# Optimization experiments

Measured on AMD Instinct MI355X. Metric: run time of the kernel, lower is better.

The kernel has to match this reference:

```python
import jax, jax.numpy as jnp
import numpy as np

B, T, D, H = 2048, 512, 32, 64


def _gru_layer(x, W_ih, W_hh, b_ih, b_hh):
    # x: [B, T, Din]; W_ih: [3H, Din]; W_hh: [3H, H]; gate order r, z, n (PyTorch).
    xp = jnp.einsum('btd,gd->btg', x, W_ih) + b_ih  # precompute input projections [B,T,3H]

    def step(h, xt):
        gh = h @ W_hh.T + b_hh                      # [B,3H]
        ir, iz, inn = jnp.split(xt, 3, axis=-1)
        hr, hz, hn = jnp.split(gh, 3, axis=-1)
        r = jax.nn.sigmoid(ir + hr)
        z = jax.nn.sigmoid(iz + hz)
        n = jnp.tanh(inn + r * hn)
        h_new = (1.0 - z) * n + z * h
        return h_new, h_new

    h0 = jnp.zeros((x.shape[0], W_hh.shape[1]), dtype=x.dtype)
    _, ys = jax.lax.scan(step, h0, xp.transpose(1, 0, 2))  # ys: [T,B,H]
    return ys.transpose(1, 0, 2)                           # [B,T,H]


def setup_inputs() -> dict:
    key = jax.random.key(0)
    ks = jax.random.split(key, 12)
    s_in = 1.0 / np.sqrt(H)
    u = lambda k, shp: jax.random.uniform(k, shp, jnp.float32, -s_in, s_in)
    return {
        'x': jax.random.normal(ks[0], (B, T, D), jnp.float32),
        'W_ih0': u(ks[1], (3 * H, D)),  'W_hh0': u(ks[2], (3 * H, H)),
        'b_ih0': u(ks[3], (3 * H,)),    'b_hh0': u(ks[4], (3 * H,)),
        'W_ih1': u(ks[5], (3 * H, H)),  'W_hh1': u(ks[6], (3 * H, H)),
        'b_ih1': u(ks[7], (3 * H,)),    'b_hh1': u(ks[8], (3 * H,)),
        'fc_w': u(ks[9], (1, H)),       'fc_b': u(ks[10], (1,)),
    }


def reference(x, W_ih0, W_hh0, b_ih0, b_hh0, W_ih1, W_hh1, b_ih1, b_hh1, fc_w, fc_b):
    # 2-layer GRU (eval mode: inter-layer dropout is identity) + linear head on last step.
    h1 = _gru_layer(x, W_ih0, W_hh0, b_ih0, b_hh0)   # [B,T,H]
    h2 = _gru_layer(h1, W_ih1, W_hh1, b_ih1, b_hh1)  # [B,T,H]
    out = h2[:, -1, :] @ fc_w.T + fc_b               # [B,1]
    return out[:, 0]                                  # [B]
```

## Files before the change

kernel.cpp:

```cpp
#include <hip/hip_runtime.h>

#define Bsz  2048
#define Tlen 512
#define Din  32
#define Hd   64
#define BT   16
#define HS   72
#define BUFE 2048
#define CHUNK 16
#define XSTR  2064
#define XBUFB (BT * XSTR)

typedef _Float16 half8 __attribute__((ext_vector_type(8)));
typedef float    f32x4 __attribute__((ext_vector_type(4)));

#define MFMA(a, b, c) __builtin_amdgcn_mfma_f32_16x16x32_f16((a), (b), (c), 0, 0, 0)

__device__ __forceinline__ half8 load8s(const float* p, float s) {
    half8 r;
#pragma unroll
    for (int j = 0; j < 8; ++j) r[j] = (_Float16)(p[j] * s);
    return r;
}
__device__ __forceinline__ half8 cvt8(float4 a, float4 b) {
    half8 r;
    r[0] = (_Float16)a.x; r[1] = (_Float16)a.y; r[2] = (_Float16)a.z; r[3] = (_Float16)a.w;
    r[4] = (_Float16)b.x; r[5] = (_Float16)b.y; r[6] = (_Float16)b.z; r[7] = (_Float16)b.w;
    return r;
}

__device__ __forceinline__ void gate_update(const f32x4& gr, const f32x4& gz,
                                            const f32x4& anx, const f32x4& anh,
                                            float hst[4], _Float16* dst, bool wr) {
#pragma unroll
    for (int r = 0; r < 4; ++r) {
        float Er = __builtin_amdgcn_exp2f(gr[r]);
        float rr = __builtin_amdgcn_rcpf(1.0f + Er);
        float yy = anx[r] + rr * anh[r];
        float En = __builtin_amdgcn_exp2f(yy);
        float Ez = __builtin_amdgcn_exp2f(gz[r]);
        float num = Ez * (1.0f - En) + hst[r] * (1.0f + En);
        float den = (1.0f + Ez) * (1.0f + En);
        hst[r] = num * __builtin_amdgcn_rcpf(den);
        if (wr) dst[r * HS] = (_Float16)hst[r];
    }
}

__device__ __forceinline__ void stage_chunk(const float* __restrict__ x, char* xs,
                                            int wave, int lane, int b0, int t0, int p) {
#pragma unroll
    for (int j = 0; j < 4; ++j) {
        const int g  = wave * 4 + j;
        const int b  = g >> 1;
        const int hh = g & 1;
        const float* gp = x + (size_t)(b0 + b) * (Tlen * Din) + (size_t)t0 * Din
                            + hh * 256 + lane * 4;
        char* lp = xs + p * XBUFB + b * XSTR + hh * 1024 + lane * 16;
        __builtin_amdgcn_global_load_lds(
            (const __attribute__((address_space(1))) void*)gp,
            (__attribute__((address_space(3))) void*)lp, 16, 0, 0);
    }
}

__global__ __launch_bounds__(512, 2)
void gru_fused(const float* __restrict__ x,
               const float* __restrict__ Wih0, const float* __restrict__ Whh0,
               const float* __restrict__ bih0, const float* __restrict__ bhh0,
               const float* __restrict__ Wih1, const float* __restrict__ Whh1,
               const float* __restrict__ bih1, const float* __restrict__ bhh1,
               const float* __restrict__ fcw,  const float* __restrict__ fcb,
               float* __restrict__ out)
{
    __shared__ _Float16 arena[4 * BUFE];
    __shared__ __attribute__((aligned(16))) char xstage[2 * XBUFB];
    __shared__ float hfin[BT][Hd];

    const int tid  = threadIdx.x;
    const int lane = tid & 63;
    const int wave = tid >> 6;
    const int grp  = wave >> 2;
    const int wg   = wave & 3;
    const int m    = lane & 15;
    const int quad = lane >> 4;
    const int col  = (wg << 4) + m;
    const int b0   = blockIdx.x << 4;

    for (int idx = tid; idx < 4 * BUFE; idx += 512) arena[idx] = (_Float16)0.f;

    stage_chunk(x, xstage, wave, lane, b0, 0, 0);
    stage_chunk(x, xstage, wave, lane, b0, CHUNK, 1);

    const float sRZ = -1.44269504f;
    const float sN  = -2.88539008f;

    half8 wx[2][3], wh[2][3];
    float brz0, brz1, bin_, bhn_;

    if (grp == 0) {
        wx[0][0] = load8s(Wih0 + (      col) * Din + quad * 8, sRZ);
        wx[0][1] = load8s(Wih0 + ( 64 + col) * Din + quad * 8, sRZ);
        wx[0][2] = load8s(Wih0 + (128 + col) * Din + quad * 8, sN);
#pragma unroll
        for (int kb = 0; kb < 2; ++kb) {
            wh[kb][0] = load8s(Whh0 + (      col) * Hd + kb * 32 + quad * 8, sRZ);
            wh[kb][1] = load8s(Whh0 + ( 64 + col) * Hd + kb * 32 + quad * 8, sRZ);
            wh[kb][2] = load8s(Whh0 + (128 + col) * Hd + kb * 32 + quad * 8, sN);
        }
        brz0 = sRZ * (bih0[col] + bhh0[col]);
        brz1 = sRZ * (bih0[64 + col] + bhh0[64 + col]);
        bin_ = sN * bih0[128 + col];
        bhn_ = sN * bhh0[128 + col];
    } else {
#pragma unroll
        for (int kb = 0; kb < 2; ++kb) {
            wx[kb][0] = load8s(Wih1 + (      col) * Hd + kb * 32 + quad * 8, sRZ);
            wx[kb][1] = load8s(Wih1 + ( 64 + col) * Hd + kb * 32 + quad * 8, sRZ);
            wx[kb][2] = load8s(Wih1 + (128 + col) * Hd + kb * 32 + quad * 8, sN);
            wh[kb][0] = load8s(Whh1 + (      col) * Hd + kb * 32 + quad * 8, sRZ);
            wh[kb][1] = load8s(Whh1 + ( 64 + col) * Hd + kb * 32 + quad * 8, sRZ);
            wh[kb][2] = load8s(Whh1 + (128 + col) * Hd + kb * 32 + quad * 8, sN);
        }
        brz0 = sRZ * (bih1[col] + bhh1[col]);
        brz1 = sRZ * (bih1[64 + col] + bhh1[64 + col]);
        bin_ = sN * bih1[128 + col];
        bhn_ = sN * bhh1[128 + col];
    }

    const int rdoff = m * HS + quad * 8;
    const int xroff = m * XSTR + quad * 32;
    const int wroff = (quad * 4) * HS + col;
    float hst[4] = {0.f, 0.f, 0.f, 0.f};
    float4 xa, xb;
    __syncthreads();

    if (grp == 0) {
        const char* xr = xstage + xroff;
        xa = *(const float4*)xr; xb = *(const float4*)(xr + 16);
    }

#define STEP(I, RO, WO)                                                          \
  do {                                                                           \
    if (grp == 0) {                                                              \
      half8 ax = cvt8(xa, xb);                                                   \
      const _Float16* s1 = arena + (RO) + rdoff;                                 \
      half8 ah0 = *(const half8*)s1;                                             \
      half8 ah1 = *(const half8*)(s1 + 32);                                      \
      f32x4 arx = {brz0, brz0, brz0, brz0};                                      \
      f32x4 azx = {brz1, brz1, brz1, brz1};                                      \
      f32x4 anx = {bin_, bin_, bin_, bin_};                                      \
      f32x4 arh = {0.f,0.f,0.f,0.f}, azh = {0.f,0.f,0.f,0.f};                    \
      f32x4 anh = {bhn_, bhn_, bhn_, bhn_};                                      \
      arh = MFMA(ah0, wh[0][0], arh); arh = MFMA(ah1, wh[1][0], arh);            \
      azh = MFMA(ah0, wh[0][1], azh); azh = MFMA(ah1, wh[1][1], azh);            \
      anh = MFMA(ah0, wh[0][2], anh); anh = MFMA(ah1, wh[1][2], anh);            \
      arx = MFMA(ax, wx[0][0], arx);                                             \
      azx = MFMA(ax, wx[0][1], azx);                                             \
      anx = MFMA(ax, wx[0][2], anx);                                             \
      f32x4 gr = arx + arh, gz = azx + azh;                                      \
      gate_update(gr, gz, anx, anh, hst, arena + (WO) + wroff, true);            \
      { const int nx = ((I) + 1 < Tlen) ? (I) + 1 : (I);                         \
        const char* xr = xstage + ((nx >> 4) & 1) * XBUFB + (nx & 15) * 128      \
                         + xroff;                                                \
        xa = *(const float4*)xr; xb = *(const float4*)(xr + 16); }               \
    } else {                                                                     \
      const _Float16* s1 = arena + (RO) + rdoff;                    \
      const _Float16* s2 = s1 + 2 * BUFE;                           \
      half8 ax0 = *(const half8*)s1;                                             \
      half8 ax1 = *(const half8*)(s1 + 32);                                      \
      half8 ah0 = *(const half8*)s2;                                             \
      half8 ah1 = *(const half8*)(s2 + 32);                                      \
      f32x4 arx = {brz0, brz0, brz0, brz0};                                      \
      f32x4 azx = {brz1, brz1, brz1, brz1};                                      \
      f32x4 anx = {bin_, bin_, bin_, bin_};                                      \
      f32x4 arh = {0.f,0.f,0.f,0.f}, azh = {0.f,0.f,0.f,0.f};                    \
      f32x4 anh = {bhn_, bhn_, bhn_, bhn_};                                      \
      arx = MFMA(ax0, wx[0][0], arx); arx = MFMA(ax1, wx[1][0], arx);            \
      azx = MFMA(ax0, wx[0][1], azx); azx = MFMA(ax1, wx[1][1], azx);            \
      anx = MFMA(ax0, wx[0][2], anx); anx = MFMA(ax1, wx[1][2], anx);            \
      arh = MFMA(ah0, wh[0][0], arh); arh = MFMA(ah1, wh[1][0], arh);            \
      azh = MFMA(ah0, wh[0][1], azh); azh = MFMA(ah1, wh[1][1], azh);            \
      anh = MFMA(ah0, wh[0][2], anh); anh = MFMA(ah1, wh[1][2], anh);            \
      f32x4 gr = arx + arh, gz = azx + azh;                                      \
      gate_update(gr, gz, anx, anh, hst, arena + (2 * BUFE) + (WO) + wroff,      \
                  true);                                                         \
    }                                                                            \
    __syncthreads();                                                             \
  } while (0)

    if (grp == 0) {
        half8 ax = cvt8(xa, xb);
        f32x4 gr  = {brz0, brz0, brz0, brz0};
        f32x4 gz  = {brz1, brz1, brz1, brz1};
        f32x4 anx = {bin_, bin_, bin_, bin_};
        f32x4 anh = {bhn_, bhn_, bhn_, bhn_};
        gr  = MFMA(ax, wx[0][0], gr);
        gz  = MFMA(ax, wx[0][1], gz);
        anx = MFMA(ax, wx[0][2], anx);
        gate_update(gr, gz, anx, anh, hst, arena + 0 + wroff, true);
        const char* xr = xstage + 128 + xroff;
        xa = *(const float4*)xr; xb = *(const float4*)(xr + 16);
    }
    __syncthreads();

    for (int i = 1; i + 1 < Tlen; i += 2) {
        STEP(i, 0, BUFE);
        if (((i + 1) & (CHUNK - 1)) == 0 && (i + 1) < Tlen - CHUNK)
            stage_chunk(x, xstage, wave, lane, b0, i + 1 + CHUNK,
                        (((i + 1) >> 4) + 1) & 1);
        STEP(i + 1, BUFE, 0);
    }
    STEP(Tlen - 1, 0, BUFE);

    if (grp == 1) {
        const _Float16* s1 = arena + BUFE + rdoff;
        const _Float16* s2 = s1 + 2 * BUFE;
        half8 ax0 = *(const half8*)s1;
        half8 ax1 = *(const half8*)(s1 + 32);
        half8 ah0 = *(const half8*)s2;
        half8 ah1 = *(const half8*)(s2 + 32);
        f32x4 arx = {brz0, brz0, brz0, brz0};
        f32x4 azx = {brz1, brz1, brz1, brz1};
        f32x4 anx = {bin_, bin_, bin_, bin_};
        f32x4 arh = {0.f,0.f,0.f,0.f}, azh = {0.f,0.f,0.f,0.f};
        f32x4 anh = {bhn_, bhn_, bhn_, bhn_};
        arx = MFMA(ax0, wx[0][0], arx); arx = MFMA(ax1, wx[1][0], arx);
        azx = MFMA(ax0, wx[0][1], azx); azx = MFMA(ax1, wx[1][1], azx);
        anx = MFMA(ax0, wx[0][2], anx); anx = MFMA(ax1, wx[1][2], anx);
        arh = MFMA(ah0, wh[0][0], arh); arh = MFMA(ah1, wh[1][0], arh);
        azh = MFMA(ah0, wh[0][1], azh); azh = MFMA(ah1, wh[1][1], azh);
        anh = MFMA(ah0, wh[0][2], anh); anh = MFMA(ah1, wh[1][2], anh);
        f32x4 gr = arx + arh, gz = azx + azh;
        gate_update(gr, gz, anx, anh, hst, nullptr, false);
#pragma unroll
        for (int r = 0; r < 4; ++r) hfin[quad * 4 + r][col] = hst[r];
    }
    __syncthreads();
    if (tid < BT) {
        float acc = fcb[0];
        for (int c = 0; c < Hd; ++c) acc += hfin[tid][c] * fcw[c];
        out[b0 + tid] = acc;
    }
#undef STEP
}

extern "C" void kernel_launch(void* const* d_in, const int* in_sizes, int n_in,
                              void* d_out, int out_size, void* d_ws, size_t ws_size,
                              hipStream_t stream) {
    gru_fused<<<dim3(Bsz / BT), dim3(512), 0, stream>>>(
        (const float*)d_in[0],
        (const float*)d_in[1], (const float*)d_in[2],
        (const float*)d_in[3], (const float*)d_in[4],
        (const float*)d_in[5], (const float*)d_in[6],
        (const float*)d_in[7], (const float*)d_in[8],
        (const float*)d_in[9], (const float*)d_in[10],
        (float*)d_out);
}
```

Baseline: 501.3 us.

## Transpose MFMA operands, stage x as fp16 via registers, vectorize h stores

Swaps the MFMA operand order so the weights form the A operand and activations the B operand. Each lane then owns 4 contiguous hidden units of one batch row, which lets h be written to LDS as a single half4 store instead of four strided scalar stores. Input x is now prefetched through registers one chunk ahead, converted to fp16 once and written to LDS at half the size. This replaces the async global_load_lds path and the per-step fp32-to-fp16 conversion. Biases become per-lane vectors. The trade-off is more registers held for the prefetch and synchronous global loads placed inside the recurrence loop.

```diff
diff --git a/kernel.cpp b/kernel.cpp
--- a/kernel.cpp
+++ b/kernel.cpp
@@ -8,10 +8,12 @@
 #define HS   72
 #define BUFE 2048
 #define CHUNK 16
-#define XSTR  2064
-#define XBUFB (BT * XSTR)
+#define NCHUNK (Tlen / CHUNK)
+#define XSTRH 1040
+#define XBUFB (BT * XSTRH)
 
 typedef _Float16 half8 __attribute__((ext_vector_type(8)));
+typedef _Float16 half4 __attribute__((ext_vector_type(4)));
 typedef float    f32x4 __attribute__((ext_vector_type(4)));
 
 #define MFMA(a, b, c) __builtin_amdgcn_mfma_f32_16x16x32_f16((a), (b), (c), 0, 0, 0)
@@ -32,6 +34,7 @@
 __device__ __forceinline__ void gate_update(const f32x4& gr, const f32x4& gz,
                                             const f32x4& anx, const f32x4& anh,
                                             float hst[4], _Float16* dst, bool wr) {
+    half4 pk;
 #pragma unroll
     for (int r = 0; r < 4; ++r) {
         float Er = __builtin_amdgcn_exp2f(gr[r]);
@@ -42,24 +45,9 @@
         float num = Ez * (1.0f - En) + hst[r] * (1.0f + En);
         float den = (1.0f + Ez) * (1.0f + En);
         hst[r] = num * __builtin_amdgcn_rcpf(den);
-        if (wr) dst[r * HS] = (_Float16)hst[r];
-    }
-}
-
-__device__ __forceinline__ void stage_chunk(const float* __restrict__ x, char* xs,
-                                            int wave, int lane, int b0, int t0, int p) {
-#pragma unroll
-    for (int j = 0; j < 4; ++j) {
-        const int g  = wave * 4 + j;
-        const int b  = g >> 1;
-        const int hh = g & 1;
-        const float* gp = x + (size_t)(b0 + b) * (Tlen * Din) + (size_t)t0 * Din
-                            + hh * 256 + lane * 4;
-        char* lp = xs + p * XBUFB + b * XSTR + hh * 1024 + lane * 16;
-        __builtin_amdgcn_global_load_lds(
-            (const __attribute__((address_space(1))) void*)gp,
-            (__attribute__((address_space(3))) void*)lp, 16, 0, 0);
-    }
+        pk[r] = (_Float16)hst[r];
+    }
+    if (wr) *(half4*)dst = pk;
 }
 
 __global__ __launch_bounds__(512, 2)
@@ -83,18 +71,45 @@
     const int m    = lane & 15;
     const int quad = lane >> 4;
     const int col  = (wg << 4) + m;
+    const int gc   = (wg << 4) + (quad << 2);
     const int b0   = blockIdx.x << 4;
 
     for (int idx = tid; idx < 4 * BUFE; idx += 512) arena[idx] = (_Float16)0.f;
 
-    stage_chunk(x, xstage, wave, lane, b0, 0, 0);
-    stage_chunk(x, xstage, wave, lane, b0, CHUNK, 1);
+    const int sb    = (wave << 1) + (lane >> 5);
+    const int st    = (lane & 31) >> 1;
+    const int sdh   = lane & 1;
+    const float* xgp = x + (size_t)(b0 + sb) * (Tlen * Din) + st * Din + sdh * 16;
+    const int swoff = sb * XSTRH + st * 64 + sdh * 32;
+
+    float4 xh0, xh1, xh2, xh3;
+    {
+        const float* p = xgp;
+        xh0 = *(const float4*)p;       xh1 = *(const float4*)(p + 4);
+        xh2 = *(const float4*)(p + 8); xh3 = *(const float4*)(p + 12);
+        char* wp = xstage + swoff;
+        *(half8*)wp        = cvt8(xh0, xh1);
+        *(half8*)(wp + 16) = cvt8(xh2, xh3);
+    }
+    {
+        const float* p = xgp + CHUNK * Din;
+        xh0 = *(const float4*)p;       xh1 = *(const float4*)(p + 4);
+        xh2 = *(const float4*)(p + 8); xh3 = *(const float4*)(p + 12);
+        char* wp = xstage + XBUFB + swoff;
+        *(half8*)wp        = cvt8(xh0, xh1);
+        *(half8*)(wp + 16) = cvt8(xh2, xh3);
+    }
+    {
+        const float* p = xgp + 2 * CHUNK * Din;
+        xh0 = *(const float4*)p;       xh1 = *(const float4*)(p + 4);
+        xh2 = *(const float4*)(p + 8); xh3 = *(const float4*)(p + 12);
+    }
 
     const float sRZ = -1.44269504f;
     const float sN  = -2.88539008f;
 
     half8 wx[2][3], wh[2][3];
-    float brz0, brz1, bin_, bhn_;
+    f32x4 brz0v, brz1v, binv, bhnv;
 
     if (grp == 0) {
         wx[0][0] = load8s(Wih0 + (      col) * Din + quad * 8, sRZ);
@@ -106,10 +121,13 @@
             wh[kb][1] = load8s(Whh0 + ( 64 + col) * Hd + kb * 32 + quad * 8, sRZ);
             wh[kb][2] = load8s(Whh0 + (128 + col) * Hd + kb * 32 + quad * 8, sN);
         }
-        brz0 = sRZ * (bih0[col] + bhh0[col]);
-        brz1 = sRZ * (bih0[64 + col] + bhh0[64 + col]);
-        bin_ = sN * bih0[128 + col];
-        bhn_ = sN * bhh0[128 + col];
+#pragma unroll
+        for (int r = 0; r < 4; ++r) {
+            brz0v[r] = sRZ * (bih0[gc + r] + bhh0[gc + r]);
+            brz1v[r] = sRZ * (bih0[64 + gc + r] + bhh0[64 + gc + r]);
+            binv[r]  = sN * bih0[128 + gc + r];
+            bhnv[r]  = sN * bhh0[128 + gc + r];
+        }
     } else {
 #pragma unroll
         for (int kb = 0; kb < 2; ++kb) {
@@ -120,93 +138,92 @@
             wh[kb][1] = load8s(Whh1 + ( 64 + col) * Hd + kb * 32 + quad * 8, sRZ);
             wh[kb][2] = load8s(Whh1 + (128 + col) * Hd + kb * 32 + quad * 8, sN);
         }
-        brz0 = sRZ * (bih1[col] + bhh1[col]);
-        brz1 = sRZ * (bih1[64 + col] + bhh1[64 + col]);
-        bin_ = sN * bih1[128 + col];
-        bhn_ = sN * bhh1[128 + col];
-    }
-
-    const int rdoff = m * HS + quad * 8;
-    const int xroff = m * XSTR + quad * 32;
-    const int wroff = (quad * 4) * HS + col;
+#pragma unroll
+        for (int r = 0; r < 4; ++r) {
+            brz0v[r] = sRZ * (bih1[gc + r] + bhh1[gc + r]);
+            brz1v[r] = sRZ * (bih1[64 + gc + r] + bhh1[64 + gc + r]);
+            binv[r]  = sN * bih1[128 + gc + r];
+            bhnv[r]  = sN * bhh1[128 + gc + r];
+        }
+    }
+
+    const int rdoff  = m * HS + quad * 8;
+    const int xroffH = m * XSTRH + quad * 16;
+    const int wroff  = m * HS + gc;
     float hst[4] = {0.f, 0.f, 0.f, 0.f};
-    float4 xa, xb;
+    half8 ax;
     __syncthreads();
 
-    if (grp == 0) {
-        const char* xr = xstage + xroff;
-        xa = *(const float4*)xr; xb = *(const float4*)(xr + 16);
-    }
+    if (grp == 0) ax = *(const half8*)(xstage + xroffH);
 
 #define STEP(I, RO, WO)                                                          \
   do {                                                                           \
     if (grp == 0) {                                                              \
-      half8 ax = cvt8(xa, xb);                                                   \
       const _Float16* s1 = arena + (RO) + rdoff;                                 \
-      half8 ah0 = *(const half8*)s1;                                             \
-      half8 ah1 = *(const half8*)(s1 + 32);                                      \
-      f32x4 arx = {brz0, brz0, brz0, brz0};                                      \
-      f32x4 azx = {brz1, brz1, brz1, brz1};                                      \
-      f32x4 anx = {bin_, bin_, bin_, bin_};                                      \
+      half8 bh0 = *(const half8*)s1;                                             \
+      half8 bh1 = *(const half8*)(s1 + 32);                                      \
+      f32x4 arx = brz0v, azx = brz1v, anx = binv;                                \
       f32x4 arh = {0.f,0.f,0.f,0.f}, azh = {0.f,0.f,0.f,0.f};                    \
-      f32x4 anh = {bhn_, bhn_, bhn_, bhn_};                                      \
-      arh = MFMA(ah0, wh[0][0], arh); arh = MFMA(ah1, wh[1][0], arh);            \
-      azh = MFMA(ah0, wh[0][1], azh); azh = MFMA(ah1, wh[1][1], azh);            \
-      anh = MFMA(ah0, wh[0][2], anh); anh = MFMA(ah1, wh[1][2], anh);            \
-      arx = MFMA(ax, wx[0][0], arx);                                             \
-      azx = MFMA(ax, wx[0][1], azx);                                             \
-      anx = MFMA(ax, wx[0][2], anx);                                             \
+      f32x4 anh = bhnv;                                                          \
+      arh = MFMA(wh[0][0], bh0, arh); arh = MFMA(wh[1][0], bh1, arh);            \
+      azh = MFMA(wh[0][1], bh0, azh); azh = MFMA(wh[1][1], bh1, azh);            \
+      anh = MFMA(wh[0][2], bh0, anh); anh = MFMA(wh[1][2], bh1, anh);            \
+      arx = MFMA(wx[0][0], ax, arx);                                             \
+      azx = MFMA(wx[0][1], ax, azx);                                             \
+      anx = MFMA(wx[0][2], ax, anx);                                             \
       f32x4 gr = arx + arh, gz = azx + azh;                                      \
       gate_update(gr, gz, anx, anh, hst, arena + (WO) + wroff, true);            \
       { const int nx = ((I) + 1 < Tlen) ? (I) + 1 : (I);                         \
-        const char* xr = xstage + ((nx >> 4) & 1) * XBUFB + (nx & 15) * 128      \
-                         + xroff;                                                \
-        xa = *(const float4*)xr; xb = *(const float4*)(xr + 16); }               \
+        ax = *(const half8*)(xstage + ((nx >> 4) & 1) * XBUFB                    \
+                             + (nx & 15) * 64 + xroffH); }                       \
     } else {                                                                     \
       const _Float16* s1 = arena + (RO) + rdoff;                    \
       const _Float16* s2 = s1 + 2 * BUFE;                           \
-      half8 ax0 = *(const half8*)s1;                                             \
-      half8 ax1 = *(const half8*)(s1 + 32);                                      \
-      half8 ah0 = *(const half8*)s2;                                             \
-      half8 ah1 = *(const half8*)(s2 + 32);                                      \
-      f32x4 arx = {brz0, brz0, brz0, brz0};                                      \
-      f32x4 azx = {brz1, brz1, brz1, brz1};                                      \
-      f32x4 anx = {bin_, bin_, bin_, bin_};                                      \
+      half8 bx0 = *(const half8*)s1;                                             \
+      half8 bx1 = *(const half8*)(s1 + 32);                                      \
+      half8 bh0 = *(const half8*)s2;                                             \
+      half8 bh1 = *(const half8*)(s2 + 32);                                      \
+      f32x4 arx = brz0v, azx = brz1v, anx = binv;                                \
       f32x4 arh = {0.f,0.f,0.f,0.f}, azh = {0.f,0.f,0.f,0.f};                    \
-      f32x4 anh = {bhn_, bhn_, bhn_, bhn_};                                      \
-      arx = MFMA(ax0, wx[0][0], arx); arx = MFMA(ax1, wx[1][0], arx);            \
-      azx = MFMA(ax0, wx[0][1], azx); azx = MFMA(ax1, wx[1][1], azx);            \
-      anx = MFMA(ax0, wx[0][2], anx); anx = MFMA(ax1, wx[1][2], anx);            \
-      arh = MFMA(ah0, wh[0][0], arh); arh = MFMA(ah1, wh[1][0], arh);            \
-      azh = MFMA(ah0, wh[0][1], azh); azh = MFMA(ah1, wh[1][1], azh);            \
-      anh = MFMA(ah0, wh[0][2], anh); anh = MFMA(ah1, wh[1][2], anh);            \
+      f32x4 anh = bhnv;                                                          \
+      arx = MFMA(wx[0][0], bx0, arx); arx = MFMA(wx[1][0], bx1, arx);            \
+      azx = MFMA(wx[0][1], bx0, azx); azx = MFMA(wx[1][1], bx1, azx);            \
+      anx = MFMA(wx[0][2], bx0, anx); anx = MFMA(wx[1][2], bx1, anx);            \
+      arh = MFMA(wh[0][0], bh0, arh); arh = MFMA(wh[1][0], bh1, arh);            \
+      azh = MFMA(wh[0][1], bh0, azh); azh = MFMA(wh[1][1], bh1, azh);            \
+      anh = MFMA(wh[0][2], bh0, anh); anh = MFMA(wh[1][2], bh1, anh);            \
       f32x4 gr = arx + arh, gz = azx + azh;                                      \
-      gate_update(gr, gz, anx, anh, hst, arena + (2 * BUFE) + (WO) + wroff,      \
+      gate_update(gr, gz, anx, anh, hst, arena + 2 * BUFE + (WO) + wroff,        \
                   true);                                                         \
     }                                                                            \
     __syncthreads();                                                             \
   } while (0)
 
     if (grp == 0) {
-        half8 ax = cvt8(xa, xb);
-        f32x4 gr  = {brz0, brz0, brz0, brz0};
-        f32x4 gz  = {brz1, brz1, brz1, brz1};
-        f32x4 anx = {bin_, bin_, bin_, bin_};
-        f32x4 anh = {bhn_, bhn_, bhn_, bhn_};
-        gr  = MFMA(ax, wx[0][0], gr);
-        gz  = MFMA(ax, wx[0][1], gz);
-        anx = MFMA(ax, wx[0][2], anx);
+        f32x4 gr = brz0v, gz = brz1v, anx = binv, anh = bhnv;
+        gr  = MFMA(wx[0][0], ax, gr);
+        gz  = MFMA(wx[0][1], ax, gz);
+        anx = MFMA(wx[0][2], ax, anx);
         gate_update(gr, gz, anx, anh, hst, arena + 0 + wroff, true);
-        const char* xr = xstage + 128 + xroff;
-        xa = *(const float4*)xr; xb = *(const float4*)(xr + 16);
+        ax = *(const half8*)(xstage + 1 * 64 + xroffH);
     }
     __syncthreads();
 
     for (int i = 1; i + 1 < Tlen; i += 2) {
         STEP(i, 0, BUFE);
-        if (((i + 1) & (CHUNK - 1)) == 0 && (i + 1) < Tlen - CHUNK)
-            stage_chunk(x, xstage, wave, lane, b0, i + 1 + CHUNK,
-                        (((i + 1) >> 4) + 1) & 1);
+        if (((i + 1) & (CHUNK - 1)) == 0) {
+            const int k = (i + 1) >> 4;
+            if (k + 1 < NCHUNK) {
+                char* wp = xstage + ((k + 1) & 1) * XBUFB + swoff;
+                *(half8*)wp        = cvt8(xh0, xh1);
+                *(half8*)(wp + 16) = cvt8(xh2, xh3);
+            }
+            if (k + 2 < NCHUNK) {
+                const float* p = xgp + (size_t)(k + 2) * (CHUNK * Din);
+                xh0 = *(const float4*)p;       xh1 = *(const float4*)(p + 4);
+                xh2 = *(const float4*)(p + 8); xh3 = *(const float4*)(p + 12);
+            }
+        }
         STEP(i + 1, BUFE, 0);
     }
     STEP(Tlen - 1, 0, BUFE);
@@ -214,25 +231,25 @@
     if (grp == 1) {
         const _Float16* s1 = arena + BUFE + rdoff;
         const _Float16* s2 = s1 + 2 * BUFE;
-        half8 ax0 = *(const half8*)s1;
-        half8 ax1 = *(const half8*)(s1 + 32);
-        half8 ah0 = *(const half8*)s2;
-        half8 ah1 = *(const half8*)(s2 + 32);
-        f32x4 arx = {brz0, brz0, brz0, brz0};
-        f32x4 azx = {brz1, brz1, brz1, brz1};
-        f32x4 anx = {bin_, bin_, bin_, bin_};
+        half8 bx0 = *(const half8*)s1;
+        half8 bx1 = *(const half8*)(s1 + 32);
+        half8 bh0 = *(const half8*)s2;
+        half8 bh1 = *(const half8*)(s2 + 32);
+        f32x4 arx = brz0v, azx = brz1v, anx = binv;
         f32x4 arh = {0.f,0.f,0.f,0.f}, azh = {0.f,0.f,0.f,0.f};
-        f32x4 anh = {bhn_, bhn_, bhn_, bhn_};
-        arx = MFMA(ax0, wx[0][0], arx); arx = MFMA(ax1, wx[1][0], arx);
-        azx = MFMA(ax0, wx[0][1], azx); azx = MFMA(ax1, wx[1][1], azx);
-        anx = MFMA(ax0, wx[0][2], anx); anx = MFMA(ax1, wx[1][2], anx);
-        arh = MFMA(ah0, wh[0][0], arh); arh = MFMA(ah1, wh[1][0], arh);
-        azh = MFMA(ah0, wh[0][1], azh); azh = MFMA(ah1, wh[1][1], azh);
-        anh = MFMA(ah0, wh[0][2], anh); anh = MFMA(ah1, wh[1][2], anh);
+        f32x4 anh = bhnv;
+        arx = MFMA(wx[0][0], bx0, arx); arx = MFMA(wx[1][0], bx1, arx);
+        azx = MFMA(wx[0][1], bx0, azx); azx = MFMA(wx[1][1], bx1, azx);
+        anx = MFMA(wx[0][2], bx0, anx); anx = MFMA(wx[1][2], bx1, anx);
+        arh = MFMA(wh[0][0], bh0, arh); arh = MFMA(wh[1][0], bh1, arh);
+        azh = MFMA(wh[0][1], bh0, azh); azh = MFMA(wh[1][1], bh1, azh);
+        anh = MFMA(wh[0][2], bh0, anh); anh = MFMA(wh[1][2], bh1, anh);
         f32x4 gr = arx + arh, gz = azx + azh;
         gate_update(gr, gz, anx, anh, hst, nullptr, false);
-#pragma unroll
-        for (int r = 0; r < 4; ++r) hfin[quad * 4 + r][col] = hst[r];
+        f32x4 fv;
+#pragma unroll
+        for (int r = 0; r < 4; ++r) fv[r] = hst[r];
+        *(f32x4*)(&hfin[m][gc]) = fv;
     }
     __syncthreads();
     if (tid < BT) {
```

After: 434.0 us. 13.4% less time.
